# Optimization experiments

Hardware: AMD Instinct MI355X
Metric: run time of the kernel (lower is better)

The kernel has to match this reference:

```python
import jax, jax.numpy as jnp
import numpy as np

B, D, C = 256, 128, 8000
MARGIN = 0.5
SCALE = 64.0
EPS = 1e-12  # tf.nn.l2_normalize epsilon


def _l2_normalize(x, axis):
    # Matches tf.nn.l2_normalize: x * rsqrt(max(sum(x^2), eps))
    sq = jnp.sum(x * x, axis=axis, keepdims=True)
    return x * jax.lax.rsqrt(jnp.maximum(sq, EPS))


def setup_inputs() -> dict:
    key = jax.random.key(0)
    k1, k2, k3 = jax.random.split(key, 3)
    embds = jax.random.normal(k1, (B, D), dtype=jnp.float32)
    w = jax.random.normal(k2, (D, C), dtype=jnp.float32)
    labels = jax.random.randint(k3, (B,), 0, C, dtype=jnp.int32)
    return {"embds": embds, "w": w, "labels": labels}


def reference(embds, w, labels):
    normed_embds = _l2_normalize(embds, axis=1)          # [B, D]
    normed_w = _l2_normalize(w, axis=0)                  # [D, C]
    gr_w = normed_w.T[labels]                            # gather per-label columns -> [B, D]
    # dw[b, d, c] = gr_w[b, d] - normed_w[d, c]
    dw = gr_w[:, :, None] - normed_w[None, :, :]         # [B, D, C]
    normed_dw = _l2_normalize(dw, axis=1)                # normalize over feature dim D
    win = jnp.einsum('bd,bdc->bc', normed_embds, normed_dw)
    penalties = MARGIN - jnp.minimum(MARGIN, win)        # [B, C]
    cos_t = normed_embds @ normed_w                      # [B, C]
    logits = jax.nn.softmax(SCALE * cos_t, axis=-1)
    return (logits, penalties)
```

## Files before the change

kernel.cpp:

```cpp
#include <hip/hip_runtime.h>
#include <math.h>

#define BB 256
#define DD 128
#define CC 8000
#define EPSF 1e-12f
#define SCALEF 64.0f
#define MARGINF 0.5f

__global__ __launch_bounds__(256) void prep_kernel(
    const float* __restrict__ embds, const float* __restrict__ w,
    const int* __restrict__ labels, float* __restrict__ neT,
    float* __restrict__ gT, float* __restrict__ rcol, float* __restrict__ s1) {
  int bid = blockIdx.x;
  int tid = threadIdx.x;
  if (bid < 32) {
    int c = bid * 256 + tid;
    if (c < CC) {
      float s = 0.f;
      #pragma unroll 8
      for (int d = 0; d < DD; ++d) {
        float v = w[d * CC + c];
        s = fmaf(v, v, s);
      }
      rcol[c] = rsqrtf(fmaxf(s, EPSF));
    }
  } else {
    __shared__ float red[3][2];
    int b = bid - 32;
    float e = 0.f, wl = 0.f;
    int d = tid;
    if (tid < 128) {
      int lab = labels[b];
      e = embds[b * DD + d];
      wl = w[d * CC + lab];
      float se = e * e, sw = wl * wl, sx = e * wl;
      #pragma unroll
      for (int off = 32; off; off >>= 1) {
        se += __shfl_down(se, off, 64);
        sw += __shfl_down(sw, off, 64);
        sx += __shfl_down(sx, off, 64);
      }
      if ((tid & 63) == 0) {
        int wid = tid >> 6;
        red[0][wid] = se; red[1][wid] = sw; red[2][wid] = sx;
      }
    }
    __syncthreads();
    if (tid < 128) {
      float Se = red[0][0] + red[0][1];
      float Sw = red[1][0] + red[1][1];
      float Sx = red[2][0] + red[2][1];
      float rn = rsqrtf(fmaxf(Se, EPSF));
      float rl = rsqrtf(fmaxf(Sw, EPSF));
      neT[d * BB + b] = e * rn;
      gT[d * BB + b] = wl * rl;
      if (tid == 0) s1[b] = Sx * rn * rl;
    }
  }
}

__global__ __launch_bounds__(256) void main_kernel(
    const float* __restrict__ w, const float* __restrict__ rcol,
    const float* __restrict__ neT, const float* __restrict__ gT,
    const float* __restrict__ s1, const int* __restrict__ labels,
    float* __restrict__ out) {
  __shared__ float neS[DD * 16];
  __shared__ float gS[DD * 16];
  int tid = threadIdx.x;
  int c0 = blockIdx.x * 256;
  int r0 = blockIdx.y * 16;

  {
    const float4* neT4 = (const float4*)neT;
    const float4* gT4 = (const float4*)gT;
    float4* neS4 = (float4*)neS;
    float4* gS4 = (float4*)gS;
    #pragma unroll
    for (int i4 = 0; i4 < 2; ++i4) {
      int idx = tid + i4 * 256;
      int d = idx >> 2;
      int r4 = idx & 3;
      int src = d * (BB / 4) + (r0 >> 2) + r4;
      neS4[idx] = neT4[src];
      gS4[idx] = gT4[src];
    }
  }
  __syncthreads();

  int tx = tid & 63;
  int ty = tid >> 6;
  int c = c0 + tx * 4;
  bool cok = c < CC;
  const float4* w4 = (const float4*)w;
  int wbase = (c0 >> 2) + tx;

  float accC[4][4];
  float accG[4][4];
  #pragma unroll
  for (int rr = 0; rr < 4; ++rr)
    #pragma unroll
    for (int j = 0; j < 4; ++j) { accC[rr][j] = 0.f; accG[rr][j] = 0.f; }

  #pragma unroll 8
  for (int d = 0; d < DD; ++d) {
    float4 wv = cok ? w4[d * (CC / 4) + wbase] : make_float4(0.f, 0.f, 0.f, 0.f);
    float4 a = *(const float4*)&neS[d * 16 + ty * 4];
    float4 g = *(const float4*)&gS[d * 16 + ty * 4];
    float av[4] = {a.x, a.y, a.z, a.w};
    float gv[4] = {g.x, g.y, g.z, g.w};
    float wj[4] = {wv.x, wv.y, wv.z, wv.w};
    #pragma unroll
    for (int rr = 0; rr < 4; ++rr) {
      #pragma unroll
      for (int j = 0; j < 4; ++j) {
        accC[rr][j] = fmaf(av[rr], wj[j], accC[rr][j]);
        accG[rr][j] = fmaf(gv[rr], wj[j], accG[rr][j]);
      }
    }
  }

  if (!cok) return;
  float4 rc4 = ((const float4*)rcol)[wbase];
  float rcj[4] = {rc4.x, rc4.y, rc4.z, rc4.w};
  float* pen_base = out + (size_t)BB * CC;
  #pragma unroll
  for (int rr = 0; rr < 4; ++rr) {
    int r = r0 + ty * 4 + rr;
    float s1v = s1[r];
    int lab = labels[r];
    float cosv[4], penv[4];
    #pragma unroll
    for (int j = 0; j < 4; ++j) {
      float cs = accC[rr][j] * rcj[j];
      float gw = accG[rr][j] * rcj[j];
      float win = (s1v - cs) * rsqrtf(fmaxf(2.f - 2.f * gw, EPSF));
      if (c + j == lab) win = 0.f;
      cosv[j] = cs;
      penv[j] = MARGINF - fminf(MARGINF, win);
    }
    size_t o4 = (size_t)r * (CC / 4) + wbase;
    ((float4*)out)[o4] = make_float4(cosv[0], cosv[1], cosv[2], cosv[3]);
    ((float4*)pen_base)[o4] = make_float4(penv[0], penv[1], penv[2], penv[3]);
  }
}

__global__ __launch_bounds__(512) void softmax_kernel(float* __restrict__ out) {
  __shared__ float red[8];
  int r = blockIdx.x;
  int tid = threadIdx.x;
  float4* row = (float4*)out + (size_t)r * (CC / 4);

  float4 vals[4];
  float m = -1e30f;
  #pragma unroll
  for (int k = 0; k < 4; ++k) {
    int i = tid + k * 512;
    if (i < CC / 4) {
      float4 v = row[i];
      vals[k] = v;
      m = fmaxf(m, fmaxf(fmaxf(v.x, v.y), fmaxf(v.z, v.w)));
    }
  }
  #pragma unroll
  for (int off = 1; off < 64; off <<= 1) m = fmaxf(m, __shfl_xor(m, off, 64));
  if ((tid & 63) == 0) red[tid >> 6] = m;
  __syncthreads();
  m = red[0];
  #pragma unroll
  for (int k = 1; k < 8; ++k) m = fmaxf(m, red[k]);
  __syncthreads();

  float s = 0.f;
  #pragma unroll
  for (int k = 0; k < 4; ++k) {
    int i = tid + k * 512;
    if (i < CC / 4) {
      float4 v = vals[k];
      float4 e;
      e.x = __expf(SCALEF * (v.x - m));
      e.y = __expf(SCALEF * (v.y - m));
      e.z = __expf(SCALEF * (v.z - m));
      e.w = __expf(SCALEF * (v.w - m));
      vals[k] = e;
      s += e.x + e.y + e.z + e.w;
    }
  }
  #pragma unroll
  for (int off = 1; off < 64; off <<= 1) s += __shfl_xor(s, off, 64);
  if ((tid & 63) == 0) red[tid >> 6] = s;
  __syncthreads();
  s = red[0];
  #pragma unroll
  for (int k = 1; k < 8; ++k) s += red[k];
  float inv = 1.f / s;

  #pragma unroll
  for (int k = 0; k < 4; ++k) {
    int i = tid + k * 512;
    if (i < CC / 4) {
      float4 e = vals[k];
      row[i] = make_float4(e.x * inv, e.y * inv, e.z * inv, e.w * inv);
    }
  }
}

extern "C" void kernel_launch(void* const* d_in, const int* in_sizes, int n_in,
                              void* d_out, int out_size, void* d_ws, size_t ws_size,
                              hipStream_t stream) {
  const float* embds = (const float*)d_in[0];
  const float* w = (const float*)d_in[1];
  const int* labels = (const int*)d_in[2];
  float* out = (float*)d_out;
  float* ws = (float*)d_ws;

  float* neT = ws;
  float* gT = ws + 32768;
  float* rcol = ws + 65536;
  float* s1 = ws + 73536;

  prep_kernel<<<288, 256, 0, stream>>>(embds, w, labels, neT, gT, rcol, s1);
  dim3 g3(32, 16);
  main_kernel<<<g3, 256, 0, stream>>>(w, rcol, neT, gT, s1, labels, out);
  softmax_kernel<<<256, 512, 0, stream>>>(out);
}
```

Before: 95.31 us.

## Split column-norm reduction across more blocks and load activations via scalar loads

The prep kernel's column-norm pass now runs on 250 blocks, each splitting the D reduction over 8 thread groups and combining partial sums in shared memory, instead of 32 blocks looping over all of D. The main kernel drops the shared-memory staging of normalized embeddings and gathered weights. It makes the row index wave-uniform with readfirstlane, so those values can be read straight from global memory as uniform (scalar) loads. This is meant to raise parallelism in the prep step and remove the staging barrier, at the cost of more global/scalar-cache traffic inside the inner loop.

```diff
diff --git a/kernel.cpp b/kernel.cpp
--- a/kernel.cpp
+++ b/kernel.cpp
@@ -14,20 +14,28 @@
     float* __restrict__ gT, float* __restrict__ rcol, float* __restrict__ s1) {
   int bid = blockIdx.x;
   int tid = threadIdx.x;
-  if (bid < 32) {
-    int c = bid * 256 + tid;
-    if (c < CC) {
-      float s = 0.f;
-      #pragma unroll 8
-      for (int d = 0; d < DD; ++d) {
-        float v = w[d * CC + c];
-        s = fmaf(v, v, s);
-      }
-      rcol[c] = rsqrtf(fmaxf(s, EPSF));
+  if (bid < 250) {
+    __shared__ float partial[8][32];
+    int col = tid & 31;
+    int dg = tid >> 5;
+    int c = bid * 32 + col;
+    float s = 0.f;
+    #pragma unroll
+    for (int k = 0; k < 16; ++k) {
+      float v = w[(dg * 16 + k) * CC + c];
+      s = fmaf(v, v, s);
+    }
+    partial[dg][col] = s;
+    __syncthreads();
+    if (tid < 32) {
+      float t = 0.f;
+      #pragma unroll
+      for (int k = 0; k < 8; ++k) t += partial[k][tid];
+      rcol[bid * 32 + tid] = rsqrtf(fmaxf(t, EPSF));
     }
   } else {
     __shared__ float red[3][2];
-    int b = bid - 32;
+    int b = bid - 250;
     float e = 0.f, wl = 0.f;
     int d = tid;
     if (tid < 128) {
@@ -65,35 +73,19 @@
     const float* __restrict__ neT, const float* __restrict__ gT,
     const float* __restrict__ s1, const int* __restrict__ labels,
     float* __restrict__ out) {
-  __shared__ float neS[DD * 16];
-  __shared__ float gS[DD * 16];
   int tid = threadIdx.x;
   int c0 = blockIdx.x * 256;
   int r0 = blockIdx.y * 16;
-
-  {
-    const float4* neT4 = (const float4*)neT;
-    const float4* gT4 = (const float4*)gT;
-    float4* neS4 = (float4*)neS;
-    float4* gS4 = (float4*)gS;
-    #pragma unroll
-    for (int i4 = 0; i4 < 2; ++i4) {
-      int idx = tid + i4 * 256;
-      int d = idx >> 2;
-      int r4 = idx & 3;
-      int src = d * (BB / 4) + (r0 >> 2) + r4;
-      neS4[idx] = neT4[src];
-      gS4[idx] = gT4[src];
-    }
-  }
-  __syncthreads();
-
   int tx = tid & 63;
-  int ty = tid >> 6;
+  int tyu = __builtin_amdgcn_readfirstlane(tid >> 6);
+  int rbase = r0 + tyu * 4;
+
   int c = c0 + tx * 4;
   bool cok = c < CC;
   const float4* w4 = (const float4*)w;
-  int wbase = (c0 >> 2) + tx;
+  const float4* neT4 = (const float4*)neT;
+  const float4* gT4 = (const float4*)gT;
+  int abase = rbase >> 2;
 
   float accC[4][4];
   float accG[4][4];
@@ -102,11 +94,12 @@
     #pragma unroll
     for (int j = 0; j < 4; ++j) { accC[rr][j] = 0.f; accG[rr][j] = 0.f; }
 
+  int wbase = (c0 >> 2) + tx;
   #pragma unroll 8
   for (int d = 0; d < DD; ++d) {
     float4 wv = cok ? w4[d * (CC / 4) + wbase] : make_float4(0.f, 0.f, 0.f, 0.f);
-    float4 a = *(const float4*)&neS[d * 16 + ty * 4];
-    float4 g = *(const float4*)&gS[d * 16 + ty * 4];
+    float4 a = neT4[d * (BB / 4) + abase];
+    float4 g = gT4[d * (BB / 4) + abase];
     float av[4] = {a.x, a.y, a.z, a.w};
     float gv[4] = {g.x, g.y, g.z, g.w};
     float wj[4] = {wv.x, wv.y, wv.z, wv.w};
@@ -126,7 +119,7 @@
   float* pen_base = out + (size_t)BB * CC;
   #pragma unroll
   for (int rr = 0; rr < 4; ++rr) {
-    int r = r0 + ty * 4 + rr;
+    int r = rbase + rr;
     float s1v = s1[r];
     int lab = labels[r];
     float cosv[4], penv[4];
@@ -219,7 +212,7 @@
   float* rcol = ws + 65536;
   float* s1 = ws + 73536;
 
-  prep_kernel<<<288, 256, 0, stream>>>(embds, w, labels, neT, gT, rcol, s1);
+  prep_kernel<<<506, 256, 0, stream>>>(embds, w, labels, neT, gT, rcol, s1);
   dim3 g3(32, 16);
   main_kernel<<<g3, 256, 0, stream>>>(w, rcol, neT, gT, s1, labels, out);
   softmax_kernel<<<256, 512, 0, stream>>>(out);
```

Measured after the change: 95.02 us. Within noise of the previous version (-0.3%).

## Fuse normalization prep into main kernel and drop softmax max pass

Applied to the files above, without the earlier changes.

Folds the prep kernel into the main GEMM kernel: each block recomputes embedding/label-column norms for its 16 rows and the column norms of w inside the d-loop. The softmax max-subtraction is dropped because cosines are bounded by 1, so exp(64*cos) stays within float range. Exponentials and per-block partial sums are written directly, and a light second kernel only rescales by the row sum. This removes a launch, the workspace round trip, and one read pass over the logits, at the cost of redundant per-block normalization work.

```diff
diff --git a/kernel.cpp b/kernel.cpp
--- a/kernel.cpp
+++ b/kernel.cpp
@@ -8,83 +8,50 @@
 #define SCALEF 64.0f
 #define MARGINF 0.5f
 
-__global__ __launch_bounds__(256) void prep_kernel(
+__global__ __launch_bounds__(256, 2) void fused_kernel(
     const float* __restrict__ embds, const float* __restrict__ w,
-    const int* __restrict__ labels, float* __restrict__ neT,
-    float* __restrict__ gT, float* __restrict__ rcol, float* __restrict__ s1) {
-  int bid = blockIdx.x;
-  int tid = threadIdx.x;
-  if (bid < 32) {
-    int c = bid * 256 + tid;
-    if (c < CC) {
-      float s = 0.f;
-      #pragma unroll 8
-      for (int d = 0; d < DD; ++d) {
-        float v = w[d * CC + c];
-        s = fmaf(v, v, s);
-      }
-      rcol[c] = rsqrtf(fmaxf(s, EPSF));
-    }
-  } else {
-    __shared__ float red[3][2];
-    int b = bid - 32;
-    float e = 0.f, wl = 0.f;
-    int d = tid;
-    if (tid < 128) {
-      int lab = labels[b];
-      e = embds[b * DD + d];
-      wl = w[d * CC + lab];
-      float se = e * e, sw = wl * wl, sx = e * wl;
-      #pragma unroll
-      for (int off = 32; off; off >>= 1) {
-        se += __shfl_down(se, off, 64);
-        sw += __shfl_down(sw, off, 64);
-        sx += __shfl_down(sx, off, 64);
-      }
-      if ((tid & 63) == 0) {
-        int wid = tid >> 6;
-        red[0][wid] = se; red[1][wid] = sw; red[2][wid] = sx;
-      }
-    }
-    __syncthreads();
-    if (tid < 128) {
-      float Se = red[0][0] + red[0][1];
-      float Sw = red[1][0] + red[1][1];
-      float Sx = red[2][0] + red[2][1];
-      float rn = rsqrtf(fmaxf(Se, EPSF));
-      float rl = rsqrtf(fmaxf(Sw, EPSF));
-      neT[d * BB + b] = e * rn;
-      gT[d * BB + b] = wl * rl;
-      if (tid == 0) s1[b] = Sx * rn * rl;
-    }
-  }
-}
-
-__global__ __launch_bounds__(256) void main_kernel(
-    const float* __restrict__ w, const float* __restrict__ rcol,
-    const float* __restrict__ neT, const float* __restrict__ gT,
-    const float* __restrict__ s1, const int* __restrict__ labels,
-    float* __restrict__ out) {
+    const int* __restrict__ labels, float* __restrict__ out,
+    float* __restrict__ psums) {
   __shared__ float neS[DD * 16];
   __shared__ float gS[DD * 16];
+  __shared__ float s1S[16];
+  __shared__ int labS[16];
+
   int tid = threadIdx.x;
   int c0 = blockIdx.x * 256;
   int r0 = blockIdx.y * 16;
 
   {
-    const float4* neT4 = (const float4*)neT;
-    const float4* gT4 = (const float4*)gT;
-    float4* neS4 = (float4*)neS;
-    float4* gS4 = (float4*)gS;
+    int r = tid >> 4;
+    int k = tid & 15;
+    int row = r0 + r;
+    int lab = labels[row];
+    const float4* e4 = (const float4*)(embds + row * DD + k * 8);
+    float4 ea = e4[0], eb = e4[1];
+    float ev[8] = {ea.x, ea.y, ea.z, ea.w, eb.x, eb.y, eb.z, eb.w};
+    float wl[8];
+    float se = 0.f, sw = 0.f, sx = 0.f;
     #pragma unroll
-    for (int i4 = 0; i4 < 2; ++i4) {
-      int idx = tid + i4 * 256;
-      int d = idx >> 2;
-      int r4 = idx & 3;
-      int src = d * (BB / 4) + (r0 >> 2) + r4;
-      neS4[idx] = neT4[src];
-      gS4[idx] = gT4[src];
+    for (int i = 0; i < 8; ++i) {
+      wl[i] = w[(k * 8 + i) * CC + lab];
+      se = fmaf(ev[i], ev[i], se);
+      sw = fmaf(wl[i], wl[i], sw);
+      sx = fmaf(ev[i], wl[i], sx);
     }
+    #pragma unroll
+    for (int off = 1; off < 16; off <<= 1) {
+      se += __shfl_xor(se, off, 64);
+      sw += __shfl_xor(sw, off, 64);
+      sx += __shfl_xor(sx, off, 64);
+    }
+    float rn = rsqrtf(fmaxf(se, EPSF));
+    float rl = rsqrtf(fmaxf(sw, EPSF));
+    #pragma unroll
+    for (int i = 0; i < 8; ++i) {
+      neS[(k * 8 + i) * 16 + r] = ev[i] * rn;
+      gS[(k * 8 + i) * 16 + r] = wl[i] * rl;
+    }
+    if (k == 0) { s1S[r] = sx * rn * rl; labS[r] = lab; }
   }
   __syncthreads();
 
@@ -95,12 +62,13 @@
   const float4* w4 = (const float4*)w;
   int wbase = (c0 >> 2) + tx;
 
-  float accC[4][4];
-  float accG[4][4];
+  float accC[4][4], accG[4][4], colsum[4];
   #pragma unroll
   for (int rr = 0; rr < 4; ++rr)
     #pragma unroll
     for (int j = 0; j < 4; ++j) { accC[rr][j] = 0.f; accG[rr][j] = 0.f; }
+  #pragma unroll
+  for (int j = 0; j < 4; ++j) colsum[j] = 0.f;
 
   #pragma unroll 8
   for (int d = 0; d < DD; ++d) {
@@ -111,6 +79,8 @@
     float gv[4] = {g.x, g.y, g.z, g.w};
     float wj[4] = {wv.x, wv.y, wv.z, wv.w};
     #pragma unroll
+    for (int j = 0; j < 4; ++j) colsum[j] = fmaf(wj[j], wj[j], colsum[j]);
+    #pragma unroll
     for (int rr = 0; rr < 4; ++rr) {
       #pragma unroll
       for (int j = 0; j < 4; ++j) {
@@ -120,87 +90,61 @@
     }
   }
 
-  if (!cok) return;
-  float4 rc4 = ((const float4*)rcol)[wbase];
-  float rcj[4] = {rc4.x, rc4.y, rc4.z, rc4.w};
+  float rcj[4];
+  #pragma unroll
+  for (int j = 0; j < 4; ++j) rcj[j] = rsqrtf(fmaxf(colsum[j], EPSF));
+
   float* pen_base = out + (size_t)BB * CC;
   #pragma unroll
   for (int rr = 0; rr < 4; ++rr) {
-    int r = r0 + ty * 4 + rr;
-    float s1v = s1[r];
-    int lab = labels[r];
-    float cosv[4], penv[4];
+    int lr = ty * 4 + rr;
+    int row = r0 + lr;
+    float s1v = s1S[lr];
+    int lab = labS[lr];
+    float penv[4], eo[4];
+    float psum = 0.f;
     #pragma unroll
     for (int j = 0; j < 4; ++j) {
       float cs = accC[rr][j] * rcj[j];
       float gw = accG[rr][j] * rcj[j];
       float win = (s1v - cs) * rsqrtf(fmaxf(2.f - 2.f * gw, EPSF));
       if (c + j == lab) win = 0.f;
-      cosv[j] = cs;
       penv[j] = MARGINF - fminf(MARGINF, win);
+      float e = cok ? __expf(SCALEF * cs) : 0.f;
+      eo[j] = e;
+      psum += e;
     }
-    size_t o4 = (size_t)r * (CC / 4) + wbase;
-    ((float4*)out)[o4] = make_float4(cosv[0], cosv[1], cosv[2], cosv[3]);
-    ((float4*)pen_base)[o4] = make_float4(penv[0], penv[1], penv[2], penv[3]);
+    if (cok) {
+      size_t o4 = (size_t)row * (CC / 4) + wbase;
+      ((float4*)pen_base)[o4] = make_float4(penv[0], penv[1], penv[2], penv[3]);
+      ((float4*)out)[o4] = make_float4(eo[0], eo[1], eo[2], eo[3]);
+    }
+    #pragma unroll
+    for (int off = 1; off < 64; off <<= 1) psum += __shfl_xor(psum, off, 64);
+    if (tx == 0) psums[row * 32 + blockIdx.x] = psum;
   }
 }
 
-__global__ __launch_bounds__(512) void softmax_kernel(float* __restrict__ out) {
-  __shared__ float red[8];
+__global__ __launch_bounds__(512) void scale_kernel(
+    float* __restrict__ out, const float* __restrict__ psums) {
+  __shared__ float invS;
   int r = blockIdx.x;
   int tid = threadIdx.x;
+  if (tid < 64) {
+    float p = (tid < 32) ? psums[r * 32 + tid] : 0.f;
+    #pragma unroll
+    for (int off = 1; off < 32; off <<= 1) p += __shfl_xor(p, off, 64);
+    if (tid == 0) invS = 1.f / p;
+  }
+  __syncthreads();
+  float inv = invS;
   float4* row = (float4*)out + (size_t)r * (CC / 4);
-
-  float4 vals[4];
-  float m = -1e30f;
   #pragma unroll
   for (int k = 0; k < 4; ++k) {
     int i = tid + k * 512;
     if (i < CC / 4) {
       float4 v = row[i];
-      vals[k] = v;
-      m = fmaxf(m, fmaxf(fmaxf(v.x, v.y), fmaxf(v.z, v.w)));
-    }
-  }
-  #pragma unroll
-  for (int off = 1; off < 64; off <<= 1) m = fmaxf(m, __shfl_xor(m, off, 64));
-  if ((tid & 63) == 0) red[tid >> 6] = m;
-  __syncthreads();
-  m = red[0];
-  #pragma unroll
-  for (int k = 1; k < 8; ++k) m = fmaxf(m, red[k]);
-  __syncthreads();
-
-  float s = 0.f;
-  #pragma unroll
-  for (int k = 0; k < 4; ++k) {
-    int i = tid + k * 512;
-    if (i < CC / 4) {
-      float4 v = vals[k];
-      float4 e;
-      e.x = __expf(SCALEF * (v.x - m));
-      e.y = __expf(SCALEF * (v.y - m));
-      e.z = __expf(SCALEF * (v.z - m));
-      e.w = __expf(SCALEF * (v.w - m));
-      vals[k] = e;
-      s += e.x + e.y + e.z + e.w;
-    }
-  }
-  #pragma unroll
-  for (int off = 1; off < 64; off <<= 1) s += __shfl_xor(s, off, 64);
-  if ((tid & 63) == 0) red[tid >> 6] = s;
-  __syncthreads();
-  s = red[0];
-  #pragma unroll
-  for (int k = 1; k < 8; ++k) s += red[k];
-  float inv = 1.f / s;
-
-  #pragma unroll
-  for (int k = 0; k < 4; ++k) {
-    int i = tid + k * 512;
-    if (i < CC / 4) {
-      float4 e = vals[k];
-      row[i] = make_float4(e.x * inv, e.y * inv, e.z * inv, e.w * inv);
+      row[i] = make_float4(v.x * inv, v.y * inv, v.z * inv, v.w * inv);
     }
   }
 }
@@ -212,15 +156,9 @@
   const float* w = (const float*)d_in[1];
   const int* labels = (const int*)d_in[2];
   float* out = (float*)d_out;
-  float* ws = (float*)d_ws;
+  float* psums = (float*)d_ws;
 
-  float* neT = ws;
-  float* gT = ws + 32768;
-  float* rcol = ws + 65536;
-  float* s1 = ws + 73536;
-
-  prep_kernel<<<288, 256, 0, stream>>>(embds, w, labels, neT, gT, rcol, s1);
-  dim3 g3(32, 16);
-  main_kernel<<<g3, 256, 0, stream>>>(w, rcol, neT, gT, s1, labels, out);
-  softmax_kernel<<<256, 512, 0, stream>>>(out);
+  dim3 gA(32, 16);
+  fused_kernel<<<gA, 256, 0, stream>>>(embds, w, labels, out, psums);
+  scale_kernel<<<256, 512, 0, stream>>>(out, psums);
 }
```

Measured after the change: 94.61 us. No clear change (-0.7%).
